# Performance work log

Measured on AMD Instinct MI355X. Metric: run time of the kernel, lower is better.

## Reference

```python
import jax, jax.numpy as jnp
import numpy as np

LN_EPS = 1e-5
NORM_EPS = 1e-12


def channel_layernorm(x, w, b):
    # LayerNorm over channel dim of NCHW tensor (torch permutes to NHWC; equivalent)
    mu = x.mean(axis=1, keepdims=True)
    var = x.var(axis=1, keepdims=True)
    xn = (x - mu) / jnp.sqrt(var + LN_EPS)
    return xn * w[None, :, None, None] + b[None, :, None, None]


def pconv(x, w):
    # 1x1 pointwise conv, w: (out_ch, in_ch)
    return jnp.einsum('bchw,oc->bohw', x, w)


def dwconv3(x, w):
    # depthwise 3x3, padding 1; w: (ch, 1, 3, 3)
    return jax.lax.conv_general_dilated(
        x, w, window_strides=(1, 1), padding='SAME',
        feature_group_count=x.shape[1],
        dimension_numbers=('NCHW', 'OIHW', 'NCHW'))


def l2norm(x):
    n = jnp.sqrt(jnp.sum(x * x, axis=-1, keepdims=True))
    return x / jnp.maximum(n, NORM_EPS)


def setup_inputs() -> dict:
    key = jax.random.key(0)
    ks = jax.random.split(key, 8)
    B, C, H, W = 4, 128, 128, 128
    NH, G = 8, 2

    def w(k, shape, fan_in):
        return jax.random.normal(k, shape, dtype=jnp.float32) * (fan_in ** -0.5)

    return {
        'x': jax.random.normal(ks[0], (B, C, H, W), dtype=jnp.float32),
        'ln1_w': jnp.ones((C,), jnp.float32),
        'ln1_b': jnp.zeros((C,), jnp.float32),
        'temperature': jnp.ones((NH, 1, 1), jnp.float32),
        'qkv_p_w': w(ks[1], (3 * C, C), C),
        'qkv_d_w': w(ks[2], (3 * C, 1, 3, 3), 9),
        'proj_w': w(ks[3], (C, C), C),
        'ln2_w': jnp.ones((C,), jnp.float32),
        'ln2_b': jnp.zeros((C,), jnp.float32),
        'g1_w': w(ks[4], (2 * G * C, C), C),
        'gd_w': w(ks[5], (2 * G * C, 1, 3, 3), 9),
        'g2_w': w(ks[6], (C, G * C), G * C),
        'num_heads': NH,
    }


def reference(x, ln1_w, ln1_b, temperature, qkv_p_w, qkv_d_w, proj_w,
              ln2_w, ln2_b, g1_w, gd_w, g2_w, num_heads):
    b, c, h, w_ = x.shape
    d = c // num_heads

    # --- MDTA branch ---
    y = channel_layernorm(x, ln1_w, ln1_b)
    qkv = dwconv3(pconv(y, qkv_p_w), qkv_d_w)  # (b, 3c, h, w)
    q, k, v = jnp.split(qkv, 3, axis=1)
    q = l2norm(q.reshape(b, num_heads, d, h * w_))
    k = l2norm(k.reshape(b, num_heads, d, h * w_))
    v = v.reshape(b, num_heads, d, h * w_)
    # transposed (channel) attention: (b, heads, d, d)
    attn = jnp.einsum('bhdn,bhen->bhde', q, k) * temperature[None]
    attn = jax.nn.softmax(attn, axis=-1)
    out = jnp.einsum('bhde,bhen->bhdn', attn, v).reshape(b, c, h, w_)
    x = x + pconv(out, proj_w)

    # --- GDFN branch ---
    y = channel_layernorm(x, ln2_w, ln2_b)
    hdn = dwconv3(pconv(y, g1_w), gd_w)  # (b, 2*gamma*c, h, w)
    x1, x2 = jnp.split(hdn, 2, axis=1)
    g = jax.nn.gelu(x1, approximate=False) * x2
    x = x + pconv(g, g2_w)
    return x
```

## Files before the change

### kernel.cpp

```cpp
#include <hip/hip_runtime.h>
#include <cstdint>
#include <cstddef>

typedef float f32x4 __attribute__((ext_vector_type(4)));
typedef __bf16 bf16x8 __attribute__((ext_vector_type(8)));

__device__ __forceinline__ float b2f(unsigned short u) {
    union { unsigned int i; float f; } z; z.i = ((unsigned int)u) << 16; return z.f;
}
__device__ __forceinline__ unsigned short f2b(float f) {
    union { float f; unsigned int i; } z; z.f = f;
    unsigned int x = z.i;
    return (unsigned short)((x + 0x7FFFu + ((x >> 16) & 1u)) >> 16);
}

static constexpr int C = 128;
static constexpr int NP = 16384;
static constexpr int NH = 8;

struct Ptr11 { const float* p[11]; };
__constant__ int kWN[11]   = {128, 128, 8, 49152, 3456, 16384, 128, 128, 65536, 4608, 32768};
__constant__ int kWOff[11] = {0, 128, 256, 272, 49424, 52880, 69264, 69392, 69520, 135056, 139664};
static constexpr int kWTotal = 172432;

__global__ __launch_bounds__(256)
void cvt_w_kernel(Ptr11 P, unsigned short* __restrict__ dst)
{
    int seg = blockIdx.y;
    int n = kWN[seg];
    int i = blockIdx.x * 256 + threadIdx.x;
    if (i >= n) return;
    dst[kWOff[seg] + i] = f2b(P.p[seg][i]);
}

__global__ __launch_bounds__(256)
void ln_kernel(const float* __restrict__ x, const unsigned short* __restrict__ g,
               const unsigned short* __restrict__ beta, unsigned short* __restrict__ y)
{
    int wave = threadIdx.x >> 6;
    int lane = threadIdx.x & 63;
    int px   = lane & 15;
    int cgrp = lane >> 4;
    int pglob = blockIdx.x * 64 + wave * 16 + px;
    int b = pglob >> 14;
    int n = pglob & (NP - 1);
    const float* xb = x + (size_t)b * C * NP + n;

    float vals[32];
    float s = 0.f, s2 = 0.f;
    #pragma unroll
    for (int i = 0; i < 32; ++i) {
        float v = xb[(size_t)(cgrp + 4 * i) * NP];
        vals[i] = v;
        s += v; s2 += v * v;
    }
    s  += __shfl_xor(s, 16, 64);  s2 += __shfl_xor(s2, 16, 64);
    s  += __shfl_xor(s, 32, 64);  s2 += __shfl_xor(s2, 32, 64);
    float mu = s * (1.0f / C);
    float var = s2 * (1.0f / C) - mu * mu;
    float rs = rsqrtf(fmaxf(var, 0.f) + 1e-5f);

    unsigned short* yb = y + (size_t)b * C * NP + n;
    #pragma unroll
    for (int i = 0; i < 32; ++i) {
        int c = cgrp + 4 * i;
        float o = (vals[i] - mu) * rs * b2f(g[c]) + b2f(beta[c]);
        yb[(size_t)c * NP] = f2b(o);
    }
}

template <int K, int EPI>
__global__ __launch_bounds__(256)
void gemm_pconv(const unsigned short* __restrict__ W,
                const unsigned short* __restrict__ X,
                void* __restrict__ Out,
                const float* __restrict__ Res,
                int Cout)
{
    __shared__ unsigned short Bs[32][128];
    const int tid = threadIdx.x;
    const int b = blockIdx.z;
    const int n0 = blockIdx.x * 128;
    const int m0 = blockIdx.y * 128;
    const unsigned short* Xb = X + (size_t)b * K * NP;
    const int wid = tid >> 6;
    const int lane = tid & 63;
    const int ln16 = lane & 15;
    const int quad = lane >> 4;
    const int wy = wid >> 1;
    const int wx = wid & 1;

    f32x4 acc[4][4];
    #pragma unroll
    for (int i = 0; i < 4; ++i)
        #pragma unroll
        for (int j = 0; j < 4; ++j)
            acc[i][j] = f32x4{0.f, 0.f, 0.f, 0.f};

    for (int k0 = 0; k0 < K; k0 += 32) {
        #pragma unroll
        for (int r = 0; r < 2; ++r) {
            int flat = tid + r * 256;
            int kk = flat >> 4;
            int nn = (flat & 15) * 8;
            uint4 v = *(const uint4*)(Xb + (size_t)(k0 + kk) * NP + n0 + nn);
            *(uint4*)(&Bs[kk][nn]) = v;
        }
        __syncthreads();

        bf16x8 afr[4];
        #pragma unroll
        for (int mt = 0; mt < 4; ++mt) {
            int m = m0 + wy * 64 + mt * 16 + ln16;
            uint4 v = *(const uint4*)(W + (size_t)m * K + k0 + quad * 8);
            afr[mt] = *(bf16x8*)&v;
        }
        bf16x8 bfr[4];
        #pragma unroll
        for (int nt = 0; nt < 4; ++nt) {
            int n = wx * 64 + nt * 16 + ln16;
            union { bf16x8 v; unsigned short u[8]; } tmp;
            #pragma unroll
            for (int j = 0; j < 8; ++j) tmp.u[j] = Bs[quad * 8 + j][n];
            bfr[nt] = tmp.v;
        }
        #pragma unroll
        for (int mt = 0; mt < 4; ++mt)
            #pragma unroll
            for (int nt = 0; nt < 4; ++nt)
                acc[mt][nt] = __builtin_amdgcn_mfma_f32_16x16x32_bf16(
                    afr[mt], bfr[nt], acc[mt][nt], 0, 0, 0);
        __syncthreads();
    }

    size_t outbase = (size_t)b * Cout * NP;
    #pragma unroll
    for (int mt = 0; mt < 4; ++mt) {
        #pragma unroll
        for (int nt = 0; nt < 4; ++nt) {
            int co0 = m0 + wy * 64 + mt * 16 + quad * 4;
            int n = n0 + wx * 64 + nt * 16 + ln16;
            #pragma unroll
            for (int r = 0; r < 4; ++r) {
                float v = acc[mt][nt][r];
                size_t idx = outbase + (size_t)(co0 + r) * NP + n;
                if (EPI == 0) ((unsigned short*)Out)[idx] = f2b(v);
                else          ((float*)Out)[idx] = Res[idx] + v;
            }
        }
    }
}

__global__ __launch_bounds__(256)
void dwconv3_kernel(const unsigned short* __restrict__ in,
                    const unsigned short* __restrict__ w9,
                    unsigned short* __restrict__ out, int CH)
{
    int t = blockIdx.x * 256 + threadIdx.x;
    int xi = (t & 15) * 8;
    int y  = (t >> 4) & 127;
    int bc = t >> 11;
    int c  = bc % CH;
    const unsigned short* base = in + (size_t)bc * NP + y * 128 + xi;

    float wr[9];
    #pragma unroll
    for (int i = 0; i < 9; ++i) wr[i] = b2f(w9[c * 9 + i]);

    uint4 rv0 = uint4{0,0,0,0}, rv1, rv2 = uint4{0,0,0,0};
    if (y > 0)   rv0 = *(const uint4*)(base - 128);
    rv1 = *(const uint4*)(base);
    if (y < 127) rv2 = *(const uint4*)(base + 128);
    uint4 rows[3] = {rv0, rv1, rv2};

    float o[8];
    #pragma unroll
    for (int j = 0; j < 8; ++j) o[j] = 0.f;

    #pragma unroll
    for (int r = 0; r < 3; ++r) {
        union { uint4 v; unsigned short u[8]; } cv; cv.v = rows[r];
        int lh = __shfl_up((int)cv.u[7], 1, 16);
        int rh = __shfl_down((int)cv.u[0], 1, 16);
        float p[10];
        p[0] = (xi > 0)   ? b2f((unsigned short)lh) : 0.f;
        p[9] = (xi < 120) ? b2f((unsigned short)rh) : 0.f;
        #pragma unroll
        for (int j = 0; j < 8; ++j) p[j + 1] = b2f(cv.u[j]);
        #pragma unroll
        for (int j = 0; j < 8; ++j)
            o[j] += wr[r * 3] * p[j] + wr[r * 3 + 1] * p[j + 1] + wr[r * 3 + 2] * p[j + 2];
    }
    union { uint4 v; unsigned short u[8]; } res;
    #pragma unroll
    for (int j = 0; j < 8; ++j) res.u[j] = f2b(o[j]);
    *(uint4*)(out + (size_t)bc * NP + y * 128 + xi) = res.v;
}

__global__ __launch_bounds__(256)
void dwgelu_kernel(const unsigned short* __restrict__ hdn,
                   const unsigned short* __restrict__ w9,
                   unsigned short* __restrict__ g)
{
    int t = blockIdx.x * 256 + threadIdx.x;
    int xi = (t & 15) * 8;
    int y  = (t >> 4) & 127;
    int bc = t >> 11;
    int c  = bc & 255;
    int b  = bc >> 8;
    const unsigned short* base1 = hdn + ((size_t)b * 512 + c) * NP + y * 128 + xi;
    const unsigned short* base2 = base1 + (size_t)256 * NP;

    float w1[9], w2[9];
    #pragma unroll
    for (int i = 0; i < 9; ++i) {
        w1[i] = b2f(w9[c * 9 + i]);
        w2[i] = b2f(w9[(c + 256) * 9 + i]);
    }

    uint4 ra0 = uint4{0,0,0,0}, ra1, ra2 = uint4{0,0,0,0};
    uint4 rb0 = uint4{0,0,0,0}, rb1, rb2 = uint4{0,0,0,0};
    if (y > 0)   { ra0 = *(const uint4*)(base1 - 128); rb0 = *(const uint4*)(base2 - 128); }
    ra1 = *(const uint4*)(base1);
    rb1 = *(const uint4*)(base2);
    if (y < 127) { ra2 = *(const uint4*)(base1 + 128); rb2 = *(const uint4*)(base2 + 128); }
    uint4 rowsA[3] = {ra0, ra1, ra2};
    uint4 rowsB[3] = {rb0, rb1, rb2};

    float a1[8], a2[8];
    #pragma unroll
    for (int j = 0; j < 8; ++j) { a1[j] = 0.f; a2[j] = 0.f; }

    #pragma unroll
    for (int r = 0; r < 3; ++r) {
        union { uint4 v; unsigned short u[8]; } c1, c2;
        c1.v = rowsA[r]; c2.v = rowsB[r];
        int lh1 = __shfl_up((int)c1.u[7], 1, 16);
        int rh1 = __shfl_down((int)c1.u[0], 1, 16);
        int lh2 = __shfl_up((int)c2.u[7], 1, 16);
        int rh2 = __shfl_down((int)c2.u[0], 1, 16);
        float p1[10], p2[10];
        p1[0] = (xi > 0)   ? b2f((unsigned short)lh1) : 0.f;
        p1[9] = (xi < 120) ? b2f((unsigned short)rh1) : 0.f;
        p2[0] = (xi > 0)   ? b2f((unsigned short)lh2) : 0.f;
        p2[9] = (xi < 120) ? b2f((unsigned short)rh2) : 0.f;
        #pragma unroll
        for (int j = 0; j < 8; ++j) { p1[j + 1] = b2f(c1.u[j]); p2[j + 1] = b2f(c2.u[j]); }
        #pragma unroll
        for (int j = 0; j < 8; ++j) {
            a1[j] += w1[r * 3] * p1[j] + w1[r * 3 + 1] * p1[j + 1] + w1[r * 3 + 2] * p1[j + 2];
            a2[j] += w2[r * 3] * p2[j] + w2[r * 3 + 1] * p2[j + 1] + w2[r * 3 + 2] * p2[j + 2];
        }
    }
    union { uint4 v; unsigned short u[8]; } res;
    #pragma unroll
    for (int j = 0; j < 8; ++j) {
        float u = a1[j];
        float tt = u * (0.7978845608f + 0.0356774081f * u * u);
        float e = __expf(2.f * tt);
        float th = 1.f - 2.f / (e + 1.f);
        float ge = 0.5f * u * (1.f + th);
        res.u[j] = f2b(ge * a2[j]);
    }
    *(uint4*)(g + (size_t)bc * NP + y * 128 + xi) = res.v;
}

__global__ __launch_bounds__(256)
void sumsq_kernel(const unsigned short* __restrict__ qkv, float* __restrict__ norms)
{
    int ch = blockIdx.x;
    int b = blockIdx.y;
    const unsigned short* p = qkv + ((size_t)b * 384 + ch) * NP;
    float s = 0.f;
    for (int i = threadIdx.x * 8; i < NP; i += 2048) {
        union { uint4 v; unsigned short u[8]; } cv;
        cv.v = *(const uint4*)(p + i);
        #pragma unroll
        for (int j = 0; j < 8; ++j) { float v = b2f(cv.u[j]); s += v * v; }
    }
    #pragma unroll
    for (int o = 32; o > 0; o >>= 1) s += __shfl_down(s, o, 64);
    __shared__ float ws4[4];
    if ((threadIdx.x & 63) == 0) ws4[threadIdx.x >> 6] = s;
    __syncthreads();
    if (threadIdx.x == 0) {
        float t = ws4[0] + ws4[1] + ws4[2] + ws4[3];
        norms[b * 256 + ch] = fmaxf(sqrtf(t), 1e-12f);
    }
}

__global__ __launch_bounds__(256)
void gram_kernel(const unsigned short* __restrict__ qkv, float* __restrict__ Spart)
{
    int h = blockIdx.x, b = blockIdx.y, sp = blockIdx.z;
    int wid = threadIdx.x >> 6, lane = threadIdx.x & 63;
    int ln16 = lane & 15, quad = lane >> 4;
    int nbase = sp * 2048 + wid * 512;
    const unsigned short* qp = qkv + ((size_t)b * 384 + h * 16 + ln16) * NP;
    const unsigned short* kp = qkv + ((size_t)b * 384 + 128 + h * 16 + ln16) * NP;
    f32x4 acc = f32x4{0.f, 0.f, 0.f, 0.f};
    for (int i = 0; i < 512; i += 32) {
        int n = nbase + i + quad * 8;
        uint4 av = *(const uint4*)(qp + n);
        uint4 bv = *(const uint4*)(kp + n);
        acc = __builtin_amdgcn_mfma_f32_16x16x32_bf16(*(bf16x8*)&av, *(bf16x8*)&bv, acc, 0, 0, 0);
    }
    float* Sp = Spart + (((size_t)(b * NH + h) * 32) + sp * 4 + wid) * 256;
    #pragma unroll
    for (int r = 0; r < 4; ++r)
        Sp[(quad * 4 + r) * 16 + ln16] = acc[r];
}

__global__ __launch_bounds__(256)
void softmax_kernel(const float* __restrict__ Spart, const float* __restrict__ norms,
                    const unsigned short* __restrict__ temp, float* __restrict__ P)
{
    int bh = blockIdx.x;
    int b = bh >> 3, h = bh & 7;
    int t = threadIdx.x;
    int dq = t >> 4, dk = t & 15;
    float sacc = 0.f;
    const float* Sp = Spart + (size_t)bh * 32 * 256;
    #pragma unroll
    for (int j = 0; j < 32; ++j) sacc += Sp[j * 256 + t];
    float nq = norms[b * 256 + h * 16 + dq];
    float nk = norms[b * 256 + 128 + h * 16 + dk];
    float v = sacc / (nq * nk) * b2f(temp[h]);
    float m = v;
    #pragma unroll
    for (int o = 8; o > 0; o >>= 1) m = fmaxf(m, __shfl_xor(m, o, 16));
    float e = __expf(v - m);
    float s = e;
    #pragma unroll
    for (int o = 8; o > 0; o >>= 1) s += __shfl_xor(s, o, 16);
    P[(size_t)bh * 256 + t] = e / s;
}

__global__ __launch_bounds__(256)
void attnv_kernel(const float* __restrict__ P, const unsigned short* __restrict__ qkv,
                  unsigned short* __restrict__ out)
{
    __shared__ float Ps[256];
    int h = blockIdx.y, b = blockIdx.z;
    Ps[threadIdx.x] = P[((size_t)b * NH + h) * 256 + threadIdx.x];
    __syncthreads();
    int n = (blockIdx.x * 256 + threadIdx.x) * 4;
    const unsigned short* vp = qkv + ((size_t)b * 384 + 256 + h * 16) * NP + n;
    float o[16][4];
    #pragma unroll
    for (int d = 0; d < 16; ++d)
        #pragma unroll
        for (int j = 0; j < 4; ++j) o[d][j] = 0.f;
    #pragma unroll
    for (int e = 0; e < 16; ++e) {
        union { uint2 v; unsigned short u[4]; } cv;
        cv.v = *(const uint2*)(vp + (size_t)e * NP);
        float v0 = b2f(cv.u[0]), v1 = b2f(cv.u[1]), v2 = b2f(cv.u[2]), v3 = b2f(cv.u[3]);
        #pragma unroll
        for (int d = 0; d < 16; ++d) {
            float p = Ps[d * 16 + e];
            o[d][0] += p * v0; o[d][1] += p * v1; o[d][2] += p * v2; o[d][3] += p * v3;
        }
    }
    unsigned short* op = out + ((size_t)b * C + h * 16) * NP + n;
    #pragma unroll
    for (int d = 0; d < 16; ++d) {
        union { uint2 v; unsigned short u[4]; } res;
        #pragma unroll
        for (int j = 0; j < 4; ++j) res.u[j] = f2b(o[d][j]);
        *(uint2*)(op + (size_t)d * NP) = res.v;
    }
}

struct Bufs {
    float* xmid;
    unsigned short* y;
    unsigned short* big;
    unsigned short* mid;
    float* norms;
    float* Spart;
    float* P;
};

static void run_pipeline(const float* x_f32, float* out_f32,
                         const unsigned short* w,
                         const Bufs& B, int nb, hipStream_t stream)
{
    const unsigned short* ln1_w   = w + 0;
    const unsigned short* ln1_b   = w + 128;
    const unsigned short* temp    = w + 256;
    const unsigned short* qkv_p_w = w + 272;
    const unsigned short* qkv_d_w = w + 49424;
    const unsigned short* proj_w  = w + 52880;
    const unsigned short* ln2_w   = w + 69264;
    const unsigned short* ln2_b   = w + 69392;
    const unsigned short* g1_w    = w + 69520;
    const unsigned short* gd_w    = w + 135056;
    const unsigned short* g2_w    = w + 139664;

    ln_kernel<<<nb * NP / 64, 256, 0, stream>>>(x_f32, ln1_w, ln1_b, B.y);
    gemm_pconv<128, 0><<<dim3(NP / 128, 3, nb), 256, 0, stream>>>(qkv_p_w, B.y, B.big, nullptr, 384);
    dwconv3_kernel<<<nb * 384 * NP / 2048, 256, 0, stream>>>(B.big, qkv_d_w, B.mid, 384);
    sumsq_kernel<<<dim3(256, nb), 256, 0, stream>>>(B.mid, B.norms);
    gram_kernel<<<dim3(NH, nb, 8), 256, 0, stream>>>(B.mid, B.Spart);
    softmax_kernel<<<nb * NH, 256, 0, stream>>>(B.Spart, B.norms, temp, B.P);
    attnv_kernel<<<dim3(NP / 1024, NH, nb), 256, 0, stream>>>(B.P, B.mid, B.y);
    gemm_pconv<128, 1><<<dim3(NP / 128, 1, nb), 256, 0, stream>>>(proj_w, B.y, B.xmid, x_f32, 128);

    ln_kernel<<<nb * NP / 64, 256, 0, stream>>>(B.xmid, ln2_w, ln2_b, B.y);
    gemm_pconv<128, 0><<<dim3(NP / 128, 4, nb), 256, 0, stream>>>(g1_w, B.y, B.big, nullptr, 512);
    dwgelu_kernel<<<nb * 256 * NP / 2048, 256, 0, stream>>>(B.big, gd_w, B.mid);
    gemm_pconv<256, 1><<<dim3(NP / 128, 1, nb), 256, 0, stream>>>(g2_w, B.mid, out_f32, B.xmid, 128);
}

extern "C" void kernel_launch(void* const* d_in, const int* in_sizes, int n_in,
                              void* d_out, int out_size, void* d_ws, size_t ws_size,
                              hipStream_t stream)
{
    (void)in_sizes; (void)n_in; (void)out_size;
    const float* x = (const float*)d_in[0];
    char* ws = (char*)d_ws;

    size_t off = 0;
    unsigned short* wpack = (unsigned short*)(ws + off);
    off += (size_t)kWTotal * 2;
    off = (off + 255) & ~(size_t)255;
    size_t header = off;

    auto layout = [&](int nb, size_t o, Bufs& B) -> size_t {
        B.xmid = (float*)(ws + o);           o += (size_t)nb * C * NP * 4;
        B.y    = (unsigned short*)(ws + o);  o += (size_t)nb * C * NP * 2;
        B.big  = (unsigned short*)(ws + o);  o += (size_t)nb * 512 * NP * 2;
        B.mid  = (unsigned short*)(ws + o);  o += (size_t)nb * 384 * NP * 2;
        B.norms = (float*)(ws + o);          o += (size_t)nb * 256 * 4;
        B.Spart = (float*)(ws + o);          o += (size_t)nb * NH * 32 * 256 * 4;
        B.P     = (float*)(ws + o);          o += (size_t)nb * NH * 256 * 4;
        return o;
    };

    Ptr11 P;
    for (int i = 0; i < 11; ++i) P.p[i] = (const float*)d_in[i + 1];
    cvt_w_kernel<<<dim3(256, 11), 256, 0, stream>>>(P, wpack);

    Bufs Bfull;
    size_t need_full = layout(4, header, Bfull);

    if (ws_size >= need_full) {
        run_pipeline(x, (float*)d_out, wpack, Bfull, 4, stream);
    } else {
        Bufs B1;
        layout(1, header, B1);
        for (int b = 0; b < 4; ++b) {
            run_pipeline(x + (size_t)b * C * NP,
                         (float*)d_out + (size_t)b * C * NP,
                         wpack, B1, 1, stream);
        }
    }
}
```

Measured before the change: 276.4 us.

## Fuse layernorms into pointwise GEMMs and merge norm sums into gram kernel

LayerNorm 1 is folded into the QKV pointwise GEMM: each block normalizes its 128-pixel tile into shared memory, then loops over all output-channel tiles. The projection GEMM now also adds the residual and computes LayerNorm 2 in its epilogue, writing a normalized bf16 copy for the next GEMM. The q/k sum-of-squares pass is merged into the gram kernel. This removes two standalone layernorm passes and one extra read of q/k. In exchange there are fewer, larger blocks (one per pixel tile instead of one per tile and channel group), which may lower occupancy and parallelism.

```diff
diff --git a/kernel.cpp b/kernel.cpp
--- a/kernel.cpp
+++ b/kernel.cpp
@@ -33,39 +33,256 @@
     dst[kWOff[seg] + i] = f2b(P.p[seg][i]);
 }
 
-__global__ __launch_bounds__(256)
-void ln_kernel(const float* __restrict__ x, const unsigned short* __restrict__ g,
-               const unsigned short* __restrict__ beta, unsigned short* __restrict__ y)
-{
-    int wave = threadIdx.x >> 6;
-    int lane = threadIdx.x & 63;
-    int px   = lane & 15;
-    int cgrp = lane >> 4;
-    int pglob = blockIdx.x * 64 + wave * 16 + px;
-    int b = pglob >> 14;
-    int n = pglob & (NP - 1);
-    const float* xb = x + (size_t)b * C * NP + n;
-
-    float vals[32];
-    float s = 0.f, s2 = 0.f;
-    #pragma unroll
-    for (int i = 0; i < 32; ++i) {
-        float v = xb[(size_t)(cgrp + 4 * i) * NP];
-        vals[i] = v;
-        s += v; s2 += v * v;
-    }
-    s  += __shfl_xor(s, 16, 64);  s2 += __shfl_xor(s2, 16, 64);
-    s  += __shfl_xor(s, 32, 64);  s2 += __shfl_xor(s2, 32, 64);
-    float mu = s * (1.0f / C);
-    float var = s2 * (1.0f / C) - mu * mu;
-    float rs = rsqrtf(fmaxf(var, 0.f) + 1e-5f);
-
-    unsigned short* yb = y + (size_t)b * C * NP + n;
-    #pragma unroll
-    for (int i = 0; i < 32; ++i) {
-        int c = cgrp + 4 * i;
-        float o = (vals[i] - mu) * rs * b2f(g[c]) + b2f(beta[c]);
-        yb[(size_t)c * NP] = f2b(o);
+template <int COUT>
+__device__ __forceinline__ void gemm_core_128(
+    const unsigned short (*Bs)[128],
+    const unsigned short* __restrict__ W,
+    unsigned short* __restrict__ OutB,
+    int n0, int tid)
+{
+    const int lane = tid & 63;
+    const int wid  = tid >> 6;
+    const int ln16 = lane & 15, quad = lane >> 4;
+    const int wy = wid >> 1, wx = wid & 1;
+    for (int cc = 0; cc < COUT / 128; ++cc) {
+        const int m0 = cc * 128;
+        f32x4 acc[4][4];
+        #pragma unroll
+        for (int i = 0; i < 4; ++i)
+            #pragma unroll
+            for (int j = 0; j < 4; ++j) acc[i][j] = f32x4{0.f, 0.f, 0.f, 0.f};
+
+        #pragma unroll
+        for (int k0 = 0; k0 < 128; k0 += 32) {
+            bf16x8 afr[4], bfr[4];
+            #pragma unroll
+            for (int mt = 0; mt < 4; ++mt) {
+                int m = m0 + wy * 64 + mt * 16 + ln16;
+                uint4 v = *(const uint4*)(W + (size_t)m * 128 + k0 + quad * 8);
+                afr[mt] = *(bf16x8*)&v;
+            }
+            #pragma unroll
+            for (int nt = 0; nt < 4; ++nt) {
+                int n = wx * 64 + nt * 16 + ln16;
+                union { bf16x8 v; unsigned short u[8]; } tmp;
+                #pragma unroll
+                for (int j = 0; j < 8; ++j) tmp.u[j] = Bs[k0 + quad * 8 + j][n];
+                bfr[nt] = tmp.v;
+            }
+            #pragma unroll
+            for (int mt = 0; mt < 4; ++mt)
+                #pragma unroll
+                for (int nt = 0; nt < 4; ++nt)
+                    acc[mt][nt] = __builtin_amdgcn_mfma_f32_16x16x32_bf16(
+                        afr[mt], bfr[nt], acc[mt][nt], 0, 0, 0);
+        }
+        #pragma unroll
+        for (int mt = 0; mt < 4; ++mt)
+            #pragma unroll
+            for (int nt = 0; nt < 4; ++nt) {
+                int co0 = m0 + wy * 64 + mt * 16 + quad * 4;
+                int n = n0 + wx * 64 + nt * 16 + ln16;
+                #pragma unroll
+                for (int r = 0; r < 4; ++r)
+                    OutB[(size_t)(co0 + r) * NP + n] = f2b(acc[mt][nt][r]);
+            }
+    }
+}
+
+template <int COUT>
+__global__ __launch_bounds__(256)
+void lngemm_kernel(const float* __restrict__ x,
+                   const unsigned short* __restrict__ lg,
+                   const unsigned short* __restrict__ lb,
+                   const unsigned short* __restrict__ W,
+                   unsigned short* __restrict__ Out)
+{
+    __shared__ unsigned short Bs[128][128];
+    __shared__ float Ssum[8][128], Ssq[8][128], Mu[128], Rs[128];
+    const int tid = threadIdx.x;
+    const int b = blockIdx.y;
+    const int n0 = blockIdx.x * 128;
+    const int pxg = tid & 31;
+    const int cseg = tid >> 5;
+    const float* xb = x + (size_t)b * C * NP + n0 + pxg * 4;
+
+    f32x4 hv[16];
+    f32x4 vs = f32x4{0.f, 0.f, 0.f, 0.f}, vq = f32x4{0.f, 0.f, 0.f, 0.f};
+    #pragma unroll
+    for (int i = 0; i < 16; ++i) {
+        f32x4 v = *(const f32x4*)(xb + (size_t)(cseg * 16 + i) * NP);
+        hv[i] = v; vs += v; vq += v * v;
+    }
+    #pragma unroll
+    for (int j = 0; j < 4; ++j) {
+        Ssum[cseg][pxg * 4 + j] = vs[j];
+        Ssq[cseg][pxg * 4 + j]  = vq[j];
+    }
+    __syncthreads();
+    if (tid < 128) {
+        float s = 0.f, q = 0.f;
+        #pragma unroll
+        for (int e = 0; e < 8; ++e) { s += Ssum[e][tid]; q += Ssq[e][tid]; }
+        float mu = s * (1.f / 128.f);
+        float var = q * (1.f / 128.f) - mu * mu;
+        Mu[tid] = mu;
+        Rs[tid] = rsqrtf(fmaxf(var, 0.f) + 1e-5f);
+    }
+    __syncthreads();
+    f32x4 mu4 = *(const f32x4*)(&Mu[pxg * 4]);
+    f32x4 rs4 = *(const f32x4*)(&Rs[pxg * 4]);
+    #pragma unroll
+    for (int i = 0; i < 16; ++i) {
+        int c = cseg * 16 + i;
+        float gw = b2f(lg[c]), bw = b2f(lb[c]);
+        union { uint2 v; unsigned short u[4]; } o;
+        #pragma unroll
+        for (int j = 0; j < 4; ++j)
+            o.u[j] = f2b((hv[i][j] - mu4[j]) * rs4[j] * gw + bw);
+        *(uint2*)(&Bs[c][pxg * 4]) = o.v;
+    }
+    __syncthreads();
+    gemm_core_128<COUT>(Bs, W, Out + (size_t)b * COUT * NP, n0, tid);
+}
+
+template <int COUT>
+__global__ __launch_bounds__(256)
+void gemm_bf16_kernel(const unsigned short* __restrict__ W,
+                      const unsigned short* __restrict__ X,
+                      unsigned short* __restrict__ Out)
+{
+    __shared__ unsigned short Bs[128][128];
+    const int tid = threadIdx.x;
+    const int b = blockIdx.y;
+    const int n0 = blockIdx.x * 128;
+    const unsigned short* Xb = X + (size_t)b * 128 * NP;
+    #pragma unroll
+    for (int r = 0; r < 8; ++r) {
+        int flat = tid + r * 256;
+        int kk = flat >> 4, nn = (flat & 15) * 8;
+        *(uint4*)(&Bs[kk][nn]) = *(const uint4*)(Xb + (size_t)kk * NP + n0 + nn);
+    }
+    __syncthreads();
+    gemm_core_128<COUT>(Bs, W, Out + (size_t)b * COUT * NP, n0, tid);
+}
+
+__global__ __launch_bounds__(256)
+void projln_kernel(const unsigned short* __restrict__ W,
+                   const unsigned short* __restrict__ Xin,
+                   const float* __restrict__ Res,
+                   float* __restrict__ Xmid,
+                   const unsigned short* __restrict__ lg,
+                   const unsigned short* __restrict__ lb,
+                   unsigned short* __restrict__ Y2)
+{
+    __shared__ unsigned short Bs[128][128];
+    __shared__ float RedS[2][128], RedQ[2][128], Mu[128], Rs[128];
+    const int tid = threadIdx.x;
+    const int b = blockIdx.y;
+    const int n0 = blockIdx.x * 128;
+    const unsigned short* Xb = Xin + (size_t)b * 128 * NP;
+    #pragma unroll
+    for (int r = 0; r < 8; ++r) {
+        int flat = tid + r * 256;
+        int kk = flat >> 4, nn = (flat & 15) * 8;
+        *(uint4*)(&Bs[kk][nn]) = *(const uint4*)(Xb + (size_t)kk * NP + n0 + nn);
+    }
+    __syncthreads();
+
+    const int lane = tid & 63, wid = tid >> 6;
+    const int ln16 = lane & 15, quad = lane >> 4;
+    const int wy = wid >> 1, wx = wid & 1;
+
+    f32x4 acc[4][4];
+    #pragma unroll
+    for (int i = 0; i < 4; ++i)
+        #pragma unroll
+        for (int j = 0; j < 4; ++j) acc[i][j] = f32x4{0.f, 0.f, 0.f, 0.f};
+
+    #pragma unroll
+    for (int k0 = 0; k0 < 128; k0 += 32) {
+        bf16x8 afr[4], bfr[4];
+        #pragma unroll
+        for (int mt = 0; mt < 4; ++mt) {
+            int m = wy * 64 + mt * 16 + ln16;
+            uint4 v = *(const uint4*)(W + (size_t)m * 128 + k0 + quad * 8);
+            afr[mt] = *(bf16x8*)&v;
+        }
+        #pragma unroll
+        for (int nt = 0; nt < 4; ++nt) {
+            int n = wx * 64 + nt * 16 + ln16;
+            union { bf16x8 v; unsigned short u[8]; } tmp;
+            #pragma unroll
+            for (int j = 0; j < 8; ++j) tmp.u[j] = Bs[k0 + quad * 8 + j][n];
+            bfr[nt] = tmp.v;
+        }
+        #pragma unroll
+        for (int mt = 0; mt < 4; ++mt)
+            #pragma unroll
+            for (int nt = 0; nt < 4; ++nt)
+                acc[mt][nt] = __builtin_amdgcn_mfma_f32_16x16x32_bf16(
+                    afr[mt], bfr[nt], acc[mt][nt], 0, 0, 0);
+    }
+
+    size_t base = (size_t)b * 128 * NP;
+    float ps[4] = {0.f, 0.f, 0.f, 0.f}, pq[4] = {0.f, 0.f, 0.f, 0.f};
+    #pragma unroll
+    for (int mt = 0; mt < 4; ++mt)
+        #pragma unroll
+        for (int nt = 0; nt < 4; ++nt) {
+            int co0 = wy * 64 + mt * 16 + quad * 4;
+            int n = n0 + wx * 64 + nt * 16 + ln16;
+            #pragma unroll
+            for (int r = 0; r < 4; ++r) {
+                size_t idx = base + (size_t)(co0 + r) * NP + n;
+                float t = Res[idx] + acc[mt][nt][r];
+                Xmid[idx] = t;
+                acc[mt][nt][r] = t;
+                ps[nt] += t; pq[nt] += t * t;
+            }
+        }
+    #pragma unroll
+    for (int nt = 0; nt < 4; ++nt) {
+        ps[nt] += __shfl_xor(ps[nt], 16, 64); ps[nt] += __shfl_xor(ps[nt], 32, 64);
+        pq[nt] += __shfl_xor(pq[nt], 16, 64); pq[nt] += __shfl_xor(pq[nt], 32, 64);
+    }
+    if (quad == 0) {
+        #pragma unroll
+        for (int nt = 0; nt < 4; ++nt) {
+            int nn = wx * 64 + nt * 16 + ln16;
+            RedS[wy][nn] = ps[nt]; RedQ[wy][nn] = pq[nt];
+        }
+    }
+    __syncthreads();
+    if (tid < 128) {
+        float s = RedS[0][tid] + RedS[1][tid];
+        float q = RedQ[0][tid] + RedQ[1][tid];
+        float mu = s * (1.f / 128.f);
+        float var = q * (1.f / 128.f) - mu * mu;
+        Mu[tid] = mu; Rs[tid] = rsqrtf(fmaxf(var, 0.f) + 1e-5f);
+    }
+    __syncthreads();
+
+    #pragma unroll
+    for (int mt = 0; mt < 4; ++mt) {
+        int co0 = wy * 64 + mt * 16 + quad * 4;
+        union { uint2 v; unsigned short u[4]; } gv, bv;
+        gv.v = *(const uint2*)(lg + co0);
+        bv.v = *(const uint2*)(lb + co0);
+        float gw[4], bw[4];
+        #pragma unroll
+        for (int r = 0; r < 4; ++r) { gw[r] = b2f(gv.u[r]); bw[r] = b2f(bv.u[r]); }
+        #pragma unroll
+        for (int nt = 0; nt < 4; ++nt) {
+            int nn = wx * 64 + nt * 16 + ln16;
+            float mu = Mu[nn], rs = Rs[nn];
+            int n = n0 + nn;
+            #pragma unroll
+            for (int r = 0; r < 4; ++r) {
+                size_t idx = base + (size_t)(co0 + r) * NP + n;
+                Y2[idx] = f2b((acc[mt][nt][r] - mu) * rs * gw[r] + bw[r]);
+            }
+        }
     }
 }
 
@@ -266,31 +483,8 @@
 }
 
 __global__ __launch_bounds__(256)
-void sumsq_kernel(const unsigned short* __restrict__ qkv, float* __restrict__ norms)
-{
-    int ch = blockIdx.x;
-    int b = blockIdx.y;
-    const unsigned short* p = qkv + ((size_t)b * 384 + ch) * NP;
-    float s = 0.f;
-    for (int i = threadIdx.x * 8; i < NP; i += 2048) {
-        union { uint4 v; unsigned short u[8]; } cv;
-        cv.v = *(const uint4*)(p + i);
-        #pragma unroll
-        for (int j = 0; j < 8; ++j) { float v = b2f(cv.u[j]); s += v * v; }
-    }
-    #pragma unroll
-    for (int o = 32; o > 0; o >>= 1) s += __shfl_down(s, o, 64);
-    __shared__ float ws4[4];
-    if ((threadIdx.x & 63) == 0) ws4[threadIdx.x >> 6] = s;
-    __syncthreads();
-    if (threadIdx.x == 0) {
-        float t = ws4[0] + ws4[1] + ws4[2] + ws4[3];
-        norms[b * 256 + ch] = fmaxf(sqrtf(t), 1e-12f);
-    }
-}
-
-__global__ __launch_bounds__(256)
-void gram_kernel(const unsigned short* __restrict__ qkv, float* __restrict__ Spart)
+void gramss_kernel(const unsigned short* __restrict__ qkv,
+                   float* __restrict__ Spart, float* __restrict__ Npart)
 {
     int h = blockIdx.x, b = blockIdx.y, sp = blockIdx.z;
     int wid = threadIdx.x >> 6, lane = threadIdx.x & 63;
@@ -299,32 +493,55 @@
     const unsigned short* qp = qkv + ((size_t)b * 384 + h * 16 + ln16) * NP;
     const unsigned short* kp = qkv + ((size_t)b * 384 + 128 + h * 16 + ln16) * NP;
     f32x4 acc = f32x4{0.f, 0.f, 0.f, 0.f};
+    float qs = 0.f, ks = 0.f;
     for (int i = 0; i < 512; i += 32) {
         int n = nbase + i + quad * 8;
         uint4 av = *(const uint4*)(qp + n);
         uint4 bv = *(const uint4*)(kp + n);
+        union { uint4 v; unsigned short u[8]; } ua, ub;
+        ua.v = av; ub.v = bv;
+        #pragma unroll
+        for (int j = 0; j < 8; ++j) {
+            float qv = b2f(ua.u[j]); qs += qv * qv;
+            float kv = b2f(ub.u[j]); ks += kv * kv;
+        }
         acc = __builtin_amdgcn_mfma_f32_16x16x32_bf16(*(bf16x8*)&av, *(bf16x8*)&bv, acc, 0, 0, 0);
     }
-    float* Sp = Spart + (((size_t)(b * NH + h) * 32) + sp * 4 + wid) * 256;
+    int bh = b * NH + h;
+    float* Sp = Spart + ((size_t)bh * 32 + sp * 4 + wid) * 256;
     #pragma unroll
     for (int r = 0; r < 4; ++r)
         Sp[(quad * 4 + r) * 16 + ln16] = acc[r];
-}
-
-__global__ __launch_bounds__(256)
-void softmax_kernel(const float* __restrict__ Spart, const float* __restrict__ norms,
-                    const unsigned short* __restrict__ temp, float* __restrict__ P)
+
+    qs += __shfl_xor(qs, 16, 64); qs += __shfl_xor(qs, 32, 64);
+    ks += __shfl_xor(ks, 16, 64); ks += __shfl_xor(ks, 32, 64);
+    __shared__ float G[4][32];
+    if (quad == 0) { G[wid][ln16] = qs; G[wid][16 + ln16] = ks; }
+    __syncthreads();
+    if (threadIdx.x < 32) {
+        float s = G[0][threadIdx.x] + G[1][threadIdx.x] + G[2][threadIdx.x] + G[3][threadIdx.x];
+        Npart[((size_t)bh * 8 + sp) * 32 + threadIdx.x] = s;
+    }
+}
+
+__global__ __launch_bounds__(256)
+void softmax2_kernel(const float* __restrict__ Spart, const float* __restrict__ Npart,
+                     const unsigned short* __restrict__ temp, float* __restrict__ P)
 {
     int bh = blockIdx.x;
-    int b = bh >> 3, h = bh & 7;
+    int h = bh & 7;
     int t = threadIdx.x;
     int dq = t >> 4, dk = t & 15;
     float sacc = 0.f;
     const float* Sp = Spart + (size_t)bh * 32 * 256;
     #pragma unroll
     for (int j = 0; j < 32; ++j) sacc += Sp[j * 256 + t];
-    float nq = norms[b * 256 + h * 16 + dq];
-    float nk = norms[b * 256 + 128 + h * 16 + dk];
+    const float* Np = Npart + (size_t)bh * 8 * 32;
+    float sq = 0.f, sk = 0.f;
+    #pragma unroll
+    for (int sp = 0; sp < 8; ++sp) { sq += Np[sp * 32 + dq]; sk += Np[sp * 32 + 16 + dk]; }
+    float nq = fmaxf(sqrtf(sq), 1e-12f);
+    float nk = fmaxf(sqrtf(sk), 1e-12f);
     float v = sacc / (nq * nk) * b2f(temp[h]);
     float m = v;
     #pragma unroll
@@ -375,11 +592,12 @@
 struct Bufs {
     float* xmid;
     unsigned short* y;
+    unsigned short* y2;
     unsigned short* big;
     unsigned short* mid;
-    float* norms;
     float* Spart;
     float* P;
+    float* Npart;
 };
 
 static void run_pipeline(const float* x_f32, float* out_f32,
@@ -398,17 +616,14 @@
     const unsigned short* gd_w    = w + 135056;
     const unsigned short* g2_w    = w + 139664;
 
-    ln_kernel<<<nb * NP / 64, 256, 0, stream>>>(x_f32, ln1_w, ln1_b, B.y);
-    gemm_pconv<128, 0><<<dim3(NP / 128, 3, nb), 256, 0, stream>>>(qkv_p_w, B.y, B.big, nullptr, 384);
+    lngemm_kernel<384><<<dim3(NP / 128, nb), 256, 0, stream>>>(x_f32, ln1_w, ln1_b, qkv_p_w, B.big);
     dwconv3_kernel<<<nb * 384 * NP / 2048, 256, 0, stream>>>(B.big, qkv_d_w, B.mid, 384);
-    sumsq_kernel<<<dim3(256, nb), 256, 0, stream>>>(B.mid, B.norms);
-    gram_kernel<<<dim3(NH, nb, 8), 256, 0, stream>>>(B.mid, B.Spart);
-    softmax_kernel<<<nb * NH, 256, 0, stream>>>(B.Spart, B.norms, temp, B.P);
+    gramss_kernel<<<dim3(NH, nb, 8), 256, 0, stream>>>(B.mid, B.Spart, B.Npart);
+    softmax2_kernel<<<nb * NH, 256, 0, stream>>>(B.Spart, B.Npart, temp, B.P);
     attnv_kernel<<<dim3(NP / 1024, NH, nb), 256, 0, stream>>>(B.P, B.mid, B.y);
-    gemm_pconv<128, 1><<<dim3(NP / 128, 1, nb), 256, 0, stream>>>(proj_w, B.y, B.xmid, x_f32, 128);
-
-    ln_kernel<<<nb * NP / 64, 256, 0, stream>>>(B.xmid, ln2_w, ln2_b, B.y);
-    gemm_pconv<128, 0><<<dim3(NP / 128, 4, nb), 256, 0, stream>>>(g1_w, B.y, B.big, nullptr, 512);
+    projln_kernel<<<dim3(NP / 128, nb), 256, 0, stream>>>(proj_w, B.y, x_f32, B.xmid, ln2_w, ln2_b, B.y2);
+
+    gemm_bf16_kernel<512><<<dim3(NP / 128, nb), 256, 0, stream>>>(g1_w, B.y2, B.big);
     dwgelu_kernel<<<nb * 256 * NP / 2048, 256, 0, stream>>>(B.big, gd_w, B.mid);
     gemm_pconv<256, 1><<<dim3(NP / 128, 1, nb), 256, 0, stream>>>(g2_w, B.mid, out_f32, B.xmid, 128);
 }
@@ -430,11 +645,12 @@
     auto layout = [&](int nb, size_t o, Bufs& B) -> size_t {
         B.xmid = (float*)(ws + o);           o += (size_t)nb * C * NP * 4;
         B.y    = (unsigned short*)(ws + o);  o += (size_t)nb * C * NP * 2;
+        B.y2   = (unsigned short*)(ws + o);  o += (size_t)nb * C * NP * 2;
         B.big  = (unsigned short*)(ws + o);  o += (size_t)nb * 512 * NP * 2;
         B.mid  = (unsigned short*)(ws + o);  o += (size_t)nb * 384 * NP * 2;
-        B.norms = (float*)(ws + o);          o += (size_t)nb * 256 * 4;
         B.Spart = (float*)(ws + o);          o += (size_t)nb * NH * 32 * 256 * 4;
         B.P     = (float*)(ws + o);          o += (size_t)nb * NH * 256 * 4;
+        B.Npart = (float*)(ws + o);          o += (size_t)nb * NH * 8 * 32 * 4;
         return o;
     };
 
```

After: 265.9 us. 1.04x faster.
